# Kernel tuning notes

Hardware: AMD Instinct MI355X
Metric: run time of the kernel (lower is better)

Reference implementation:

```python
import jax, jax.numpy as jnp
import numpy as np
import itertools

NUM_VARS = 8
HID = 128
NLAYERS = 2
B = 8192

PAIRS = np.array(list(itertools.combinations(range(NUM_VARS), 2)), dtype=np.int32)    # [28,2]
TRIPS = np.array(list(itertools.combinations(range(NUM_VARS), 3)), dtype=np.int32)   # [56,3]


def _make_params(key, n, d_in):
    ks = jax.random.split(key, 6)
    s_in = 1.0 / np.sqrt(d_in)
    s_h = 1.0 / np.sqrt(HID)
    return dict(
        W_in=jax.random.uniform(ks[0], (n, HID, d_in), minval=-s_in, maxval=s_in),
        b_in=jax.random.uniform(ks[1], (n, HID), minval=-s_in, maxval=s_in),
        W_h=jax.random.uniform(ks[2], (n, NLAYERS, HID, HID), minval=-s_h, maxval=s_h),
        b_h=jax.random.uniform(ks[3], (n, NLAYERS, HID), minval=-s_h, maxval=s_h),
        W_out=jax.random.uniform(ks[4], (n, 1, HID), minval=-s_h, maxval=s_h),
        b_out=jax.random.uniform(ks[5], (n,), minval=-s_h, maxval=s_h),
    )


def setup_inputs() -> dict:
    key = jax.random.key(0)
    kx, k1, k2, k3 = jax.random.split(key, 4)
    p1 = _make_params(k1, NUM_VARS, 1)
    p2 = _make_params(k2, len(PAIRS), 2)
    p3 = _make_params(k3, len(TRIPS), 3)
    inp = {"x": jax.random.normal(kx, (B, NUM_VARS), dtype=jnp.float32),
           "f0": jnp.float32(0.0)}
    for tag, p in (("1", p1), ("2", p2), ("3", p3)):
        for name, v in p.items():
            inp[f"{name}_{tag}"] = v
    return inp


def _grouped_mlp(inp, W_in, b_in, W_h, b_h, W_out, b_out):
    # inp: [n, B, d_in] -> [n, B]; one sigmoid-MLP per group n, batched.
    out = jax.nn.sigmoid(jnp.einsum('nbi,nhi->nbh', inp, W_in) + b_in[:, None, :])
    for l in range(W_h.shape[1]):
        out = jax.nn.sigmoid(jnp.einsum('nbh,ngh->nbg', out, W_h[:, l]) + b_h[:, l, None, :])
    return jnp.einsum('nbh,noh->nbo', out, W_out)[..., 0] + b_out[:, None]


def reference(x, f0,
              W_in_1, b_in_1, W_h_1, b_h_1, W_out_1, b_out_1,
              W_in_2, b_in_2, W_h_2, b_h_2, W_out_2, b_out_2,
              W_in_3, b_in_3, W_h_3, b_h_3, W_out_3, b_out_3):
    f0_out = f0 * jnp.ones_like(x[:, 0])                       # [B]

    # first order: inputs [n1, B, 1]
    in1 = x.T[:, :, None]
    f_j = _grouped_mlp(in1, W_in_1, b_in_1, W_h_1, b_h_1, W_out_1, b_out_1) - f0_out[None]  # [n1,B]

    # second order: [n2, B, 2]
    in2 = jnp.transpose(x[:, PAIRS], (1, 0, 2))
    f_jj = (_grouped_mlp(in2, W_in_2, b_in_2, W_h_2, b_h_2, W_out_2, b_out_2)
            - f_j[PAIRS[:, 0]] - f_j[PAIRS[:, 1]] - f0_out[None])  # [n2,B]

    # third order: [n3, B, 3]; NOTE: faithfully indexes f_jj by VARIABLE indices
    # (as the original code does), not by pair index.
    in3 = jnp.transpose(x[:, TRIPS], (1, 0, 2))
    i3, j3, k3 = TRIPS[:, 0], TRIPS[:, 1], TRIPS[:, 2]
    f_jjj = (_grouped_mlp(in3, W_in_3, b_in_3, W_h_3, b_h_3, W_out_3, b_out_3)
             - f_jj[i3] - f_jj[j3] - f_jj[k3]
             - f_j[i3] - f_j[j3] - f_j[k3] - f0_out[None])        # [n3,B]

    final = f0_out + f_j.sum(0) + f_jj.sum(0) + f_jjj.sum(0)      # [B]
    return final[:, None]                                         # [B,1]
```

## Files before the change

kernel.cpp:

```cpp
#include <hip/hip_runtime.h>

#define HID 128
#define BM 128
#define NT 512
#define TPB 4
#define GRPS 16
#define NNET 92
#define NBLK (NNET * GRPS)
#define LOG2E 1.44269504f

typedef _Float16 f16;
typedef _Float16 f16x2 __attribute__((ext_vector_type(2)));
typedef _Float16 f16x4 __attribute__((ext_vector_type(4)));
typedef _Float16 f16x8 __attribute__((ext_vector_type(8)));
typedef float f32x4 __attribute__((ext_vector_type(4)));

__constant__ signed char VARS_C[NNET][3] = {
  {0,-1,-1},{1,-1,-1},{2,-1,-1},{3,-1,-1},{4,-1,-1},{5,-1,-1},{6,-1,-1},{7,-1,-1},
  {0,1,-1},{0,2,-1},{0,3,-1},{0,4,-1},{0,5,-1},{0,6,-1},{0,7,-1},
  {1,2,-1},{1,3,-1},{1,4,-1},{1,5,-1},{1,6,-1},{1,7,-1},
  {2,3,-1},{2,4,-1},{2,5,-1},{2,6,-1},{2,7,-1},
  {3,4,-1},{3,5,-1},{3,6,-1},{3,7,-1},
  {4,5,-1},{4,6,-1},{4,7,-1},
  {5,6,-1},{5,7,-1},
  {6,7,-1},
  {0,1,2},{0,1,3},{0,1,4},{0,1,5},{0,1,6},{0,1,7},
  {0,2,3},{0,2,4},{0,2,5},{0,2,6},{0,2,7},
  {0,3,4},{0,3,5},{0,3,6},{0,3,7},
  {0,4,5},{0,4,6},{0,4,7},
  {0,5,6},{0,5,7},
  {0,6,7},
  {1,2,3},{1,2,4},{1,2,5},{1,2,6},{1,2,7},
  {1,3,4},{1,3,5},{1,3,6},{1,3,7},
  {1,4,5},{1,4,6},{1,4,7},
  {1,5,6},{1,5,7},
  {1,6,7},
  {2,3,4},{2,3,5},{2,3,6},{2,3,7},
  {2,4,5},{2,4,6},{2,4,7},
  {2,5,6},{2,5,7},
  {2,6,7},
  {3,4,5},{3,4,6},{3,4,7},
  {3,5,6},{3,5,7},
  {3,6,7},
  {4,5,6},{4,5,7},
  {4,6,7},
  {5,6,7}
};

__constant__ float COEF_C[NNET] = {
  120.f, 15.f, 15.f, -6.f, -6.f, -6.f, -6.f, -6.f,
  -20.f,-20.f,-20.f,-20.f,-20.f,-20.f,-20.f,-20.f,
  1.f,1.f,1.f,1.f,1.f,1.f,1.f,1.f,1.f,1.f,
  1.f,1.f,1.f,1.f,1.f,1.f,1.f,1.f,1.f,1.f,
  1.f,1.f,1.f,1.f,1.f,1.f,1.f,1.f,1.f,1.f,
  1.f,1.f,1.f,1.f,1.f,1.f,1.f,1.f,1.f,1.f,
  1.f,1.f,1.f,1.f,1.f,1.f,1.f,1.f,1.f,1.f,
  1.f,1.f,1.f,1.f,1.f,1.f,1.f,1.f,1.f,1.f,
  1.f,1.f,1.f,1.f,1.f,1.f,1.f,1.f,1.f,1.f,
  1.f,1.f
};

__device__ __forceinline__ float sig2(float s) {
    return __builtin_amdgcn_rcpf(1.0f + __builtin_amdgcn_exp2f(s));
}

__device__ __forceinline__ int actoff(int row, int colbyte) {
    return row * 256 + (colbyte ^ ((row & 7) << 4));
}

#define SW 3014656
#define SO1 1024
#define SO2 3584
#define SO3 7168
#define CVT_TOTAL (SW + SO1 + SO2 + SO3)
__global__ __launch_bounds__(256)
void cvt_w(const float* __restrict__ Wh1, const float* __restrict__ Wh2,
           const float* __restrict__ Wh3, const float* __restrict__ Wo1,
           const float* __restrict__ Wo2, const float* __restrict__ Wo3,
           f16* __restrict__ dst) {
    const int i = (blockIdx.x * 256 + threadIdx.x) * 4;
    if (i >= CVT_TOTAL) return;
    float scale;
    const float* s;
    if (i < SW) {
        scale = -LOG2E;
        if (i < 262144)         s = Wh1 + i;
        else if (i < 1179648)   s = Wh2 + (i - 262144);
        else                    s = Wh3 + (i - 1179648);
    } else {
        scale = 1.0f;
        int j = i - SW;
        if (j < SO1)            s = Wo1 + j;
        else if (j < SO1 + SO2) s = Wo2 + (j - SO1);
        else                    s = Wo3 + (j - SO1 - SO2);
    }
    float4 v = *(const float4*)s;
    f16x4 h = { (f16)(scale*v.x), (f16)(scale*v.y), (f16)(scale*v.z), (f16)(scale*v.w) };
    *(f16x4*)(dst + i) = h;
}

__global__ __launch_bounds__(NT, 4)
void hdmr_fused(const float* __restrict__ x, const float* __restrict__ f0p,
    const float* __restrict__ Wi1, const float* __restrict__ bi1,
    const float* __restrict__ bh1, const float* __restrict__ bo1,
    const float* __restrict__ Wi2, const float* __restrict__ bi2,
    const float* __restrict__ bh2, const float* __restrict__ bo2,
    const float* __restrict__ Wi3, const float* __restrict__ bi3,
    const float* __restrict__ bh3, const float* __restrict__ bo3,
    const f16* __restrict__ Whf, const f16* __restrict__ WoF,
    float* __restrict__ out)
{
    __shared__ __attribute__((aligned(16))) char actb[2][BM * HID * 2];
    __shared__ __attribute__((aligned(16))) float xr[2][BM * 8];
    __shared__ float wi_s[HID][3];
    __shared__ float bi_s[HID];

    const int tid = threadIdx.x;
    const int bid = blockIdx.x;
    const int swz = (bid & 7) * (NBLK / 8) + (bid >> 3);
    const int N = swz >> 4;
    const int grp = swz & (GRPS - 1);
    const int m_base = grp * (TPB * BM);

    int din, lidx;
    const float *Wi, *bi, *bh, *bo;
    if (N < 8)       { lidx = N;      din = 1; Wi=Wi1; bi=bi1; bh=bh1; bo=bo1; }
    else if (N < 36) { lidx = N - 8;  din = 2; Wi=Wi2; bi=bi2; bh=bh2; bo=bo2; }
    else             { lidx = N - 36; din = 3; Wi=Wi3; bi=bi3; bh=bh3; bo=bo3; }
    Wi += (size_t)lidx * HID * din;
    bi += (size_t)lidx * HID;
    bh += (size_t)lidx * 2 * HID;
    const float bout = bo[lidx];
    const float coef = COEF_C[N];
    const float f0c = (N == 0) ? 35.0f * f0p[0] : 0.0f;
    const f16* WN = Whf + (size_t)N * (2 * HID * HID);

    const int lane = tid & 63;
    const int wv = tid >> 6;
    const int lr = lane & 15;
    const int lk = lane >> 4;
    const int C0 = wv * 16;

    f16x8 wA0[4], wA1[4], wOut[4];
    #pragma unroll
    for (int kt = 0; kt < 4; ++kt) {
        wA0[kt] = *(const f16x8*)(WN + (size_t)(C0 + lr) * HID + kt * 32 + lk * 8);
        wA1[kt] = *(const f16x8*)(WN + HID * HID + (size_t)(C0 + lr) * HID + kt * 32 + lk * 8);
        wOut[kt] = *(const f16x8*)(WoF + (size_t)N * HID + kt * 32 + lk * 8);
    }
    f32x4 bias0 = *(const f32x4*)(bh + C0 + lk * 4);
    f32x4 bias1 = *(const f32x4*)(bh + HID + C0 + lk * 4);
    #pragma unroll
    for (int i = 0; i < 4; ++i) { bias0[i] *= -LOG2E; bias1[i] *= -LOG2E; }

    const int v0 = VARS_C[N][0];
    const int v1 = VARS_C[N][1] < 0 ? 0 : VARS_C[N][1];
    const int v2 = VARS_C[N][2] < 0 ? 0 : VARS_C[N][2];

    if (tid < HID) {
        #pragma unroll
        for (int ii = 0; ii < 3; ++ii)
            wi_s[tid][ii] = (ii < din) ? -LOG2E * Wi[tid * din + ii] : 0.0f;
        bi_s[tid] = -LOG2E * bi[tid];
    }
    if (tid < 256)
        ((float4*)xr[0])[tid] = ((const float4*)(x + (size_t)m_base * 8))[tid];
    __syncthreads();

    f32x4 acc[8];

    for (int t = 0; t < TPB; ++t) {
        const int p = t & 1;
        f32x4 acco = (f32x4){0.f, 0.f, 0.f, 0.f};
        if (t > 0) {
            #pragma unroll
            for (int kt = 0; kt < 4; ++kt) {
                f16x8 bfr = *(const f16x8*)(actb[p ^ 1] + actoff(C0 + lr, (kt * 32 + lk * 8) * 2));
                acco = __builtin_amdgcn_mfma_f32_16x16x32_f16(wOut[kt], bfr, acco, 0, 0, 0);
            }
        }
        {
            const int r = C0 + lr;
            const float* xrow = &xr[p][r * 8];
            const float x0 = xrow[v0], x1 = xrow[v1], x2 = xrow[v2];
            #pragma unroll
            for (int q = 0; q < 16; ++q) {
                const int c = lk * 32 + q * 2;
                float sA = bi_s[c]     + x0 * wi_s[c][0]     + x1 * wi_s[c][1]     + x2 * wi_s[c][2];
                float sB = bi_s[c + 1] + x0 * wi_s[c + 1][0] + x1 * wi_s[c + 1][1] + x2 * wi_s[c + 1][2];
                f16x2 hv = { (f16)sig2(sA), (f16)sig2(sB) };
                *(f16x2*)(actb[p] + actoff(r, c * 2)) = hv;
            }
        }
        if (t > 0 && lk == 0) {
            atomicAdd(&out[m_base + (t - 1) * BM + C0 + lr], coef * (acco[0] + bout) - f0c);
        }
        __syncthreads();

        #pragma unroll
        for (int mt = 0; mt < 8; ++mt) acc[mt] = bias0;
        #pragma unroll
        for (int kt = 0; kt < 4; ++kt) {
            const int kb = (kt * 32 + lk * 8) * 2;
            #pragma unroll
            for (int mh = 0; mh < 2; ++mh) {
                f16x8 bfr[4];
                #pragma unroll
                for (int mi = 0; mi < 4; ++mi)
                    bfr[mi] = *(const f16x8*)(actb[p] + actoff((mh * 4 + mi) * 16 + lr, kb));
                #pragma unroll
                for (int mi = 0; mi < 4; ++mi)
                    acc[mh * 4 + mi] = __builtin_amdgcn_mfma_f32_16x16x32_f16(wA0[kt], bfr[mi], acc[mh * 4 + mi], 0, 0, 0);
            }
        }
        if (t + 1 < TPB && tid < 256)
            ((float4*)xr[p ^ 1])[tid] = ((const float4*)(x + (size_t)(m_base + (t + 1) * BM) * 8))[tid];
        #pragma unroll
        for (int mt = 0; mt < 8; ++mt) {
            f16x4 hv;
            #pragma unroll
            for (int i = 0; i < 4; ++i) hv[i] = (f16)sig2(acc[mt][i]);
            *(f16x4*)(actb[p ^ 1] + actoff(mt * 16 + lr, (C0 + lk * 4) * 2)) = hv;
        }
        __syncthreads();

        #pragma unroll
        for (int mt = 0; mt < 8; ++mt) acc[mt] = bias1;
        #pragma unroll
        for (int kt = 0; kt < 4; ++kt) {
            const int kb = (kt * 32 + lk * 8) * 2;
            #pragma unroll
            for (int mh = 0; mh < 2; ++mh) {
                f16x8 bfr[4];
                #pragma unroll
                for (int mi = 0; mi < 4; ++mi)
                    bfr[mi] = *(const f16x8*)(actb[p ^ 1] + actoff((mh * 4 + mi) * 16 + lr, kb));
                #pragma unroll
                for (int mi = 0; mi < 4; ++mi)
                    acc[mh * 4 + mi] = __builtin_amdgcn_mfma_f32_16x16x32_f16(wA1[kt], bfr[mi], acc[mh * 4 + mi], 0, 0, 0);
            }
        }
        #pragma unroll
        for (int mt = 0; mt < 8; ++mt) {
            f16x4 hv;
            #pragma unroll
            for (int i = 0; i < 4; ++i) hv[i] = (f16)sig2(acc[mt][i]);
            *(f16x4*)(actb[p] + actoff(mt * 16 + lr, (C0 + lk * 4) * 2)) = hv;
        }
        __syncthreads();
    }

    {
        f32x4 acco = (f32x4){0.f, 0.f, 0.f, 0.f};
        #pragma unroll
        for (int kt = 0; kt < 4; ++kt) {
            f16x8 bfr = *(const f16x8*)(actb[1] + actoff(C0 + lr, (kt * 32 + lk * 8) * 2));
            acco = __builtin_amdgcn_mfma_f32_16x16x32_f16(wOut[kt], bfr, acco, 0, 0, 0);
        }
        if (lk == 0)
            atomicAdd(&out[m_base + (TPB - 1) * BM + C0 + lr], coef * (acco[0] + bout) - f0c);
    }
}

extern "C" void kernel_launch(void* const* d_in, const int* in_sizes, int n_in,
                              void* d_out, int out_size, void* d_ws, size_t ws_size,
                              hipStream_t stream) {
    const float* x   = (const float*)d_in[0];
    const float* f0  = (const float*)d_in[1];
    const float* Wi1 = (const float*)d_in[2];
    const float* bi1 = (const float*)d_in[3];
    const float* Wh1 = (const float*)d_in[4];
    const float* bh1 = (const float*)d_in[5];
    const float* Wo1 = (const float*)d_in[6];
    const float* bo1 = (const float*)d_in[7];
    const float* Wi2 = (const float*)d_in[8];
    const float* bi2 = (const float*)d_in[9];
    const float* Wh2 = (const float*)d_in[10];
    const float* bh2 = (const float*)d_in[11];
    const float* Wo2 = (const float*)d_in[12];
    const float* bo2 = (const float*)d_in[13];
    const float* Wi3 = (const float*)d_in[14];
    const float* bi3 = (const float*)d_in[15];
    const float* Wh3 = (const float*)d_in[16];
    const float* bh3 = (const float*)d_in[17];
    const float* Wo3 = (const float*)d_in[18];
    const float* bo3 = (const float*)d_in[19];
    float* out = (float*)d_out;
    f16* Whf = (f16*)d_ws;
    f16* WoF = Whf + SW;

    hipMemsetAsync(out, 0, (size_t)out_size * sizeof(float), stream);
    hipLaunchKernelGGL(cvt_w, dim3((CVT_TOTAL / 4 + 255) / 256), dim3(256), 0, stream,
                       Wh1, Wh2, Wh3, Wo1, Wo2, Wo3, Whf);
    hipLaunchKernelGGL(hdmr_fused, dim3(NBLK), dim3(NT), 0, stream,
                       x, f0, Wi1, bi1, bh1, bo1,
                       Wi2, bi2, bh2, bo2,
                       Wi3, bi3, bh3, bo3, Whf, WoF, out);
}
```

Measured before the change: 228.9 us.

## Replace global atomics with per-network partial buffer and separate reduction kernel

Result: no change. 230.5 us (+0.7%).

```diff
diff --git a/kernel.cpp b/kernel.cpp
--- a/kernel.cpp
+++ b/kernel.cpp
@@ -8,6 +8,7 @@
 #define NNET 92
 #define NBLK (NNET * GRPS)
 #define LOG2E 1.44269504f
+#define NROWS 8192
 
 typedef _Float16 f16;
 typedef _Float16 f16x2 __attribute__((ext_vector_type(2)));
@@ -99,6 +100,19 @@
     *(f16x4*)(dst + i) = h;
 }
 
+__global__ __launch_bounds__(128)
+void reduce_out(const float* __restrict__ part, float* __restrict__ out) {
+    const int r4 = blockIdx.x * 128 + threadIdx.x;
+    const float4* p4 = (const float4*)part;
+    float4 s = p4[r4];
+    #pragma unroll 4
+    for (int n = 1; n < NNET; ++n) {
+        float4 v = p4[(size_t)n * (NROWS / 4) + r4];
+        s.x += v.x; s.y += v.y; s.z += v.z; s.w += v.w;
+    }
+    ((float4*)out)[r4] = s;
+}
+
 __global__ __launch_bounds__(NT, 4)
 void hdmr_fused(const float* __restrict__ x, const float* __restrict__ f0p,
     const float* __restrict__ Wi1, const float* __restrict__ bi1,
@@ -108,7 +122,7 @@
     const float* __restrict__ Wi3, const float* __restrict__ bi3,
     const float* __restrict__ bh3, const float* __restrict__ bo3,
     const f16* __restrict__ Whf, const f16* __restrict__ WoF,
-    float* __restrict__ out)
+    float* __restrict__ part)
 {
     __shared__ __attribute__((aligned(16))) char actb[2][BM * HID * 2];
     __shared__ __attribute__((aligned(16))) float xr[2][BM * 8];
@@ -134,6 +148,7 @@
     const float coef = COEF_C[N];
     const float f0c = (N == 0) ? 35.0f * f0p[0] : 0.0f;
     const f16* WN = Whf + (size_t)N * (2 * HID * HID);
+    float* partN = part + (size_t)N * NROWS + m_base;
 
     const int lane = tid & 63;
     const int wv = tid >> 6;
@@ -183,17 +198,21 @@
             const int r = C0 + lr;
             const float* xrow = &xr[p][r * 8];
             const float x0 = xrow[v0], x1 = xrow[v1], x2 = xrow[v2];
+            f16x8 pk[4];
             #pragma unroll
             for (int q = 0; q < 16; ++q) {
                 const int c = lk * 32 + q * 2;
                 float sA = bi_s[c]     + x0 * wi_s[c][0]     + x1 * wi_s[c][1]     + x2 * wi_s[c][2];
                 float sB = bi_s[c + 1] + x0 * wi_s[c + 1][0] + x1 * wi_s[c + 1][1] + x2 * wi_s[c + 1][2];
-                f16x2 hv = { (f16)sig2(sA), (f16)sig2(sB) };
-                *(f16x2*)(actb[p] + actoff(r, c * 2)) = hv;
+                pk[q >> 2][(q & 3) * 2]     = (f16)sig2(sA);
+                pk[q >> 2][(q & 3) * 2 + 1] = (f16)sig2(sB);
             }
+            #pragma unroll
+            for (int qq = 0; qq < 4; ++qq)
+                *(f16x8*)(actb[p] + actoff(r, (lk * 32 + qq * 8) * 2)) = pk[qq];
         }
         if (t > 0 && lk == 0) {
-            atomicAdd(&out[m_base + (t - 1) * BM + C0 + lr], coef * (acco[0] + bout) - f0c);
+            partN[(t - 1) * BM + C0 + lr] = coef * (acco[0] + bout) - f0c;
         }
         __syncthreads();
 
@@ -258,7 +277,7 @@
             acco = __builtin_amdgcn_mfma_f32_16x16x32_f16(wOut[kt], bfr, acco, 0, 0, 0);
         }
         if (lk == 0)
-            atomicAdd(&out[m_base + (TPB - 1) * BM + C0 + lr], coef * (acco[0] + bout) - f0c);
+            partN[(TPB - 1) * BM + C0 + lr] = coef * (acco[0] + bout) - f0c;
     }
 }
 
@@ -286,14 +305,17 @@
     const float* Wo3 = (const float*)d_in[18];
     const float* bo3 = (const float*)d_in[19];
     float* out = (float*)d_out;
+
     f16* Whf = (f16*)d_ws;
     f16* WoF = Whf + SW;
-
-    hipMemsetAsync(out, 0, (size_t)out_size * sizeof(float), stream);
+    float* part = (float*)(Whf + SW + 16384);
+
     hipLaunchKernelGGL(cvt_w, dim3((CVT_TOTAL / 4 + 255) / 256), dim3(256), 0, stream,
                        Wh1, Wh2, Wh3, Wo1, Wo2, Wo3, Whf);
     hipLaunchKernelGGL(hdmr_fused, dim3(NBLK), dim3(NT), 0, stream,
                        x, f0, Wi1, bi1, bh1, bo1,
                        Wi2, bi2, bh2, bo2,
-                       Wi3, bi3, bh3, bo3, Whf, WoF, out);
-}
+                       Wi3, bi3, bh3, bo3, Whf, WoF, part);
+    hipLaunchKernelGGL(reduce_out, dim3(NROWS / 4 / 128), dim3(128), 0, stream,
+                       part, out);
+}
```
